# Performance work log

Measured on AMD Instinct MI355X. Metric: run time of the kernel, lower is better.

Reference implementation:

```python
import jax, jax.numpy as jnp
import numpy as np

D_MODEL = 1024
HIDDEN = 512
NUM_EXPERTS = 16
TOP_K = 2
CAP_FACTOR = 1.25
ALPHA = 0.01


def setup_inputs() -> dict:
    key = jax.random.key(0)
    ks = jax.random.split(key, 10)
    s_in = 1.0 / np.sqrt(D_MODEL)
    s_h = 1.0 / np.sqrt(HIDDEN)
    return {
        "x": jax.random.normal(ks[0], (4, 4096, D_MODEL), dtype=jnp.float32),
        "gate_w": jax.random.normal(ks[1], (D_MODEL, NUM_EXPERTS), dtype=jnp.float32) * s_in,
        "gate_b": jnp.zeros((NUM_EXPERTS,), dtype=jnp.float32),
        "gp_w": jax.random.normal(ks[2], (NUM_EXPERTS, D_MODEL, HIDDEN), dtype=jnp.float32) * s_in,
        "gp_b": jnp.zeros((NUM_EXPERTS, HIDDEN), dtype=jnp.float32),
        "up_w": jax.random.normal(ks[3], (NUM_EXPERTS, D_MODEL, HIDDEN), dtype=jnp.float32) * s_in,
        "up_b": jnp.zeros((NUM_EXPERTS, HIDDEN), dtype=jnp.float32),
        "dp_w": jax.random.normal(ks[4], (NUM_EXPERTS, HIDDEN, D_MODEL), dtype=jnp.float32) * s_h,
        "dp_b": jnp.zeros((NUM_EXPERTS, D_MODEL), dtype=jnp.float32),
    }


def reference(x, gate_w, gate_b, gp_w, gp_b, up_w, up_b, dp_w, dp_b):
    B, S, D = x.shape
    T = B * S
    xf = x.reshape(T, D)

    # --- MoEGate ---
    logits = xf @ gate_w + gate_b                      # [T, E]
    scores = jax.nn.softmax(logits, axis=-1)
    topk_w, topk_i = jax.lax.top_k(scores, TOP_K)      # [T, K]
    # norm_topk_prob=True in DeepSeekMoE
    topk_w = topk_w / (jnp.sum(topk_w, axis=-1, keepdims=True) + 1e-9)

    one_hot = jax.nn.one_hot(topk_i, NUM_EXPERTS, dtype=jnp.float32)  # [T, K, E]
    load = jnp.sum(one_hot, axis=(0, 1))               # [E]
    capacity = CAP_FACTOR * (T * TOP_K) / NUM_EXPERTS
    capacity_penalty = jnp.sum(jax.nn.relu(load - capacity)) / NUM_EXPERTS / T
    aux_loss = ALPHA * capacity_penalty

    # combine weight of expert e for each token: [T, E]
    comb = jnp.einsum("tke,tk->te", one_hot, topk_w)

    # --- dispatch/combine (dense per-expert, weighted by comb) ---
    out = jnp.zeros_like(xf)
    for e in range(NUM_EXPERTS):
        # Expert: down_proj(gate_proj(x) * silu(up_proj(x)))
        h = (xf @ gp_w[e] + gp_b[e]) * jax.nn.silu(xf @ up_w[e] + up_b[e])
        y = h @ dp_w[e] + dp_b[e]
        out = out + comb[:, e:e + 1] * y

    return out.reshape(B, S, D), aux_loss
```

## Files before the change

### kernel.cpp

```cpp
#include <hip/hip_runtime.h>
#include <hip/hip_bf16.h>
#include <math.h>

#define T_TOK 16384
#define DMODEL 1024
#define HID 512
#define NEXP 16
#define NASSIGN (T_TOK * 2)
#define HIST_BLK 64
#define TOK_PER_BLK (T_TOK / HIST_BLK)

typedef __bf16 bf16_8 __attribute__((ext_vector_type(8)));
typedef __bf16 bf16_4 __attribute__((ext_vector_type(4)));
typedef float f32_4 __attribute__((ext_vector_type(4)));

__device__ __forceinline__ void gload16(const __bf16* g, __bf16* l) {
  __builtin_amdgcn_global_load_lds(
      (const __attribute__((address_space(1))) void*)g,
      (__attribute__((address_space(3))) void*)l, 16, 0, 0);
}

__global__ __launch_bounds__(256) void gate_compute_kernel(
    const float* __restrict__ x, const float* __restrict__ gw, const float* __restrict__ gb,
    __bf16* __restrict__ xb, int* __restrict__ topk_idx, float2* __restrict__ topk_w)
{
  __shared__ __align__(16) float gws[4 * 1024 * 4];

  int tid = threadIdx.x;
#pragma unroll
  for (int i = 0; i < 16; ++i) {
    int c = i * 256 + tid;
    f32_4 v = ((const f32_4*)gw)[c];
    ((f32_4*)gws)[((c & 3) << 10) | (c >> 2)] = v;
  }
  __syncthreads();

  int wave = tid >> 6, lane = tid & 63;
  int tbase = blockIdx.x * 32 + wave * 8;

#pragma unroll 1
  for (int pass = 0; pass < 2; ++pass) {
    int t0 = tbase + pass * 4;
    const float* xr0 = x + (size_t)t0 * DMODEL;
    const float* xr1 = xr0 + DMODEL;
    const float* xr2 = xr1 + DMODEL;
    const float* xr3 = xr2 + DMODEL;
    __bf16* xw0 = xb + (size_t)t0 * DMODEL;
    __bf16* xw1 = xw0 + DMODEL;
    __bf16* xw2 = xw1 + DMODEL;
    __bf16* xw3 = xw2 + DMODEL;

    f32_4 acc0[4], acc1[4], acc2[4], acc3[4];
    {
      f32_4 z = {0.f, 0.f, 0.f, 0.f};
#pragma unroll
      for (int g = 0; g < 4; ++g) { acc0[g] = z; acc1[g] = z; acc2[g] = z; acc3[g] = z; }
    }

#pragma unroll
    for (int j = 0; j < 16; ++j) {
      int k = j * 64 + lane;
      float xv0 = xr0[k], xv1 = xr1[k], xv2 = xr2[k], xv3 = xr3[k];
      xw0[k] = (__bf16)xv0;
      xw1[k] = (__bf16)xv1;
      xw2[k] = (__bf16)xv2;
      xw3[k] = (__bf16)xv3;
      f32_4 w0 = ((const f32_4*)gws)[k];
      f32_4 w1 = ((const f32_4*)gws)[1024 + k];
      f32_4 w2 = ((const f32_4*)gws)[2048 + k];
      f32_4 w3 = ((const f32_4*)gws)[3072 + k];
      acc0[0] += xv0 * w0; acc0[1] += xv0 * w1; acc0[2] += xv0 * w2; acc0[3] += xv0 * w3;
      acc1[0] += xv1 * w0; acc1[1] += xv1 * w1; acc1[2] += xv1 * w2; acc1[3] += xv1 * w3;
      acc2[0] += xv2 * w0; acc2[1] += xv2 * w1; acc2[2] += xv2 * w2; acc2[3] += xv2 * w3;
      acc3[0] += xv3 * w0; acc3[1] += xv3 * w1; acc3[2] += xv3 * w2; acc3[3] += xv3 * w3;
    }

#pragma unroll
    for (int g = 0; g < 4; ++g)
#pragma unroll
      for (int w = 0; w < 4; ++w) {
        float v0 = acc0[g][w], v1 = acc1[g][w], v2 = acc2[g][w], v3 = acc3[g][w];
#pragma unroll
        for (int s = 32; s; s >>= 1) {
          v0 += __shfl_xor(v0, s, 64);
          v1 += __shfl_xor(v1, s, 64);
          v2 += __shfl_xor(v2, s, 64);
          v3 += __shfl_xor(v3, s, 64);
        }
        acc0[g][w] = v0; acc1[g][w] = v1; acc2[g][w] = v2; acc3[g][w] = v3;
      }

    int ti = lane & 3;
    float sc[16];
#pragma unroll
    for (int e = 0; e < 16; ++e) {
      int g = e >> 2, w = e & 3;
      float v = ti == 0 ? acc0[g][w] : ti == 1 ? acc1[g][w] : ti == 2 ? acc2[g][w] : acc3[g][w];
      sc[e] = v + gb[e];
    }
    float mx = -1e30f;
#pragma unroll
    for (int e = 0; e < 16; ++e) mx = fmaxf(mx, sc[e]);
    float Z = 0.f;
#pragma unroll
    for (int e = 0; e < 16; ++e) { sc[e] = expf(sc[e] - mx); Z += sc[e]; }
    int i0 = 0; float s0 = sc[0];
#pragma unroll
    for (int e = 1; e < 16; ++e) if (sc[e] > s0) { s0 = sc[e]; i0 = e; }
    int i1 = -1; float s1 = -1e30f;
#pragma unroll
    for (int e = 0; e < 16; ++e) if (e != i0 && sc[e] > s1) { s1 = sc[e]; i1 = e; }
    s0 /= Z; s1 /= Z;
    float dn = s0 + s1 + 1e-9f;
    if (lane < 4) {
      int t = t0 + ti;
      topk_idx[t] = i0 | (i1 << 8);
      topk_w[t] = make_float2(s0 / dn, s1 / dn);
    }
  }
}

__global__ __launch_bounds__(256) void hist_kernel(
    const int* __restrict__ topk_idx, int* __restrict__ block_hist)
{
  __shared__ int cnt[NEXP];
  int tid = threadIdx.x;
  if (tid < NEXP) cnt[tid] = 0;
  __syncthreads();
  int t = blockIdx.x * TOK_PER_BLK + tid;
  int p = topk_idx[t];
  atomicAdd(&cnt[p & 0xff], 1);
  atomicAdd(&cnt[p >> 8], 1);
  __syncthreads();
  if (tid < NEXP) block_hist[blockIdx.x * NEXP + tid] = cnt[tid];
}

__global__ void scan2_kernel(const int* __restrict__ block_hist,
                             int* __restrict__ counts, int* __restrict__ offsets,
                             int* __restrict__ block_base, float* __restrict__ aux_out)
{
  __shared__ int cl[NEXP];
  int lane = threadIdx.x;
  if (lane < NEXP) {
    int s = 0;
    for (int b = 0; b < HIST_BLK; ++b) s += block_hist[b * NEXP + lane];
    cl[lane] = s;
    counts[lane] = s;
  }
  __syncthreads();
  if (lane < NEXP) {
    int off = 0;
    for (int e = 0; e < lane; ++e) off += cl[e];
    offsets[lane] = off;
    int base = off;
    for (int b = 0; b < HIST_BLK; ++b) {
      block_base[b * NEXP + lane] = base;
      base += block_hist[b * NEXP + lane];
    }
  }
  if (lane == 0) {
    int tot = 0; float pen = 0.f;
    const float cap = 1.25f * (float)(T_TOK * 2) / (float)NEXP;
    for (int e = 0; e < NEXP; ++e) {
      tot += cl[e];
      float ld = (float)cl[e] - cap;
      pen += ld > 0.f ? ld : 0.f;
    }
    offsets[NEXP] = tot;
    aux_out[0] = 0.01f * pen / (float)NEXP / (float)T_TOK;
  }
}

__global__ __launch_bounds__(256) void scatter_kernel(
    const int* __restrict__ topk_idx, const int* __restrict__ block_base,
    int* __restrict__ tok_list, int2* __restrict__ tok_slots)
{
  __shared__ int base[NEXP];
  int tid = threadIdx.x;
  if (tid < NEXP) base[tid] = block_base[blockIdx.x * NEXP + tid];
  __syncthreads();
  int t = blockIdx.x * TOK_PER_BLK + tid;
  int p = topk_idx[t];
  int i0 = p & 0xff, i1 = p >> 8;
  int p0 = atomicAdd(&base[i0], 1);
  tok_list[p0] = t;
  int p1 = atomicAdd(&base[i1], 1);
  tok_list[p1] = t;
  tok_slots[t] = make_int2(p0, p1);
}

__global__ __launch_bounds__(256) void transpose_w1_kernel(const float* __restrict__ gp,
                                                           const float* __restrict__ up,
                                                           __bf16* __restrict__ wb1)
{
  __shared__ float tile[32][33];
  int ez = blockIdx.z;
  int e = ez >> 1, isup = ez & 1;
  const float* in = isup ? up : gp;
  int c0 = blockIdx.x * 32, r0 = blockIdx.y * 32;
  const float* src = in + ((size_t)e * 1024 + r0) * 512 + c0;
#pragma unroll
  for (int i = 0; i < 4; ++i) {
    int r = threadIdx.y + i * 8;
    tile[r][threadIdx.x] = src[(size_t)r * 512 + threadIdx.x];
  }
  __syncthreads();
#pragma unroll
  for (int i = 0; i < 4; ++i) {
    int cc = threadIdx.y + i * 8;
    int np = 2 * c0 + 2 * (cc & ~15) + (cc & 15) + 16 * isup;
    wb1[((size_t)e * 1024 + np) * 1024 + r0 + threadIdx.x] = (__bf16)tile[threadIdx.x][cc];
  }
}

__global__ __launch_bounds__(256) void transpose_dp_kernel(const float* __restrict__ in,
                                                           __bf16* __restrict__ out)
{
  __shared__ float tile[32][33];
  int e = blockIdx.z;
  int c0 = blockIdx.x * 32, r0 = blockIdx.y * 32;
  const float* src = in + ((size_t)e * 512 + r0) * 1024 + c0;
#pragma unroll
  for (int i = 0; i < 4; ++i) {
    int r = threadIdx.y + i * 8;
    tile[r][threadIdx.x] = src[(size_t)r * 1024 + threadIdx.x];
  }
  __syncthreads();
  __bf16* dst = out + ((size_t)e * 1024 + c0) * 512 + r0;
#pragma unroll
  for (int i = 0; i < 4; ++i) {
    int c = threadIdx.y + i * 8;
    dst[(size_t)c * 512 + threadIdx.x] = (__bf16)tile[threadIdx.x][c];
  }
}


#define PHASE_MID()                                          \
  __builtin_amdgcn_sched_barrier(0);                         \
  __builtin_amdgcn_s_barrier();                              \
  asm volatile("s_waitcnt lgkmcnt(0)" ::: "memory");         \
  __builtin_amdgcn_sched_barrier(0);                         \
  __builtin_amdgcn_s_setprio(1);

#define PHASE_END()                                          \
  __builtin_amdgcn_s_setprio(0);                             \
  __builtin_amdgcn_sched_barrier(0);                         \
  __builtin_amdgcn_s_barrier();

#define KTILE_BODY(STG)                                                           \
  {                                                                               \
    const __bf16* A_ = AsL + cur * 16384;                                         \
    const __bf16* B_ = BsL + cur * 16384;                                         \
    bf16_8 af[8];                                                                 \
    bf16_8 b0, b1;                                                                \
                     \
    _Pragma("unroll")                                                             \
    for (int mi = 0; mi < 8; ++mi)                                                \
      af[mi] = *(const bf16_8*)(A_ + abase + mi * 1024 + c0);                     \
    b0 = *(const bf16_8*)(B_ + bbase + c0);                                       \
    b1 = *(const bf16_8*)(B_ + bbase + 1024 + c0);                                \
    if (STG) {                                                                    \
      gload16(ga0 + koff, AsL + nxt * 16384 + tid * 8);                           \
      gload16(ga1 + koff, AsL + nxt * 16384 + 4096 + tid * 8);                    \
      gload16(ga2 + koff, AsL + nxt * 16384 + 8192 + tid * 8);                    \
      gload16(ga3 + koff, AsL + nxt * 16384 + 12288 + tid * 8);                   \
    }                                                                             \
    PHASE_MID();                                                                  \
    _Pragma("unroll")                                                             \
    for (int mi = 0; mi < 8; ++mi) {                                              \
      acc[mi][0] = __builtin_amdgcn_mfma_f32_16x16x32_bf16(af[mi], b0, acc[mi][0], 0, 0, 0); \
      acc[mi][1] = __builtin_amdgcn_mfma_f32_16x16x32_bf16(af[mi], b1, acc[mi][1], 0, 0, 0); \
    }                                                                             \
    PHASE_END();                                                                  \
                                       \
    b0 = *(const bf16_8*)(B_ + bbase + 2048 + c0);                                \
    b1 = *(const bf16_8*)(B_ + bbase + 3072 + c0);                                \
    if (STG) {                                                                    \
      gload16(gb0 + koff, BsL + nxt * 16384 + tid * 8);                           \
      gload16(gb1 + koff, BsL + nxt * 16384 + 4096 + tid * 8);                    \
      gload16(gb2 + koff, BsL + nxt * 16384 + 8192 + tid * 8);                    \
      gload16(gb3 + koff, BsL + nxt * 16384 + 12288 + tid * 8);                   \
    }                                                                             \
    PHASE_MID();                                                                  \
    _Pragma("unroll")                                                             \
    for (int mi = 0; mi < 8; ++mi) {                                              \
      acc[mi][2] = __builtin_amdgcn_mfma_f32_16x16x32_bf16(af[mi], b0, acc[mi][2], 0, 0, 0); \
      acc[mi][3] = __builtin_amdgcn_mfma_f32_16x16x32_bf16(af[mi], b1, acc[mi][3], 0, 0, 0); \
    }                                                                             \
    PHASE_END();                                                                  \
                                     \
    _Pragma("unroll")                                                             \
    for (int mi = 0; mi < 8; ++mi)                                                \
      af[mi] = *(const bf16_8*)(A_ + abase + mi * 1024 + (c0 ^ 32));              \
    b0 = *(const bf16_8*)(B_ + bbase + (c0 ^ 32));                                \
    b1 = *(const bf16_8*)(B_ + bbase + 1024 + (c0 ^ 32));                         \
    PHASE_MID();                                                                  \
    _Pragma("unroll")                                                             \
    for (int mi = 0; mi < 8; ++mi) {                                              \
      acc[mi][0] = __builtin_amdgcn_mfma_f32_16x16x32_bf16(af[mi], b0, acc[mi][0], 0, 0, 0); \
      acc[mi][1] = __builtin_amdgcn_mfma_f32_16x16x32_bf16(af[mi], b1, acc[mi][1], 0, 0, 0); \
    }                                                                             \
    PHASE_END();                                                                  \
          \
    b0 = *(const bf16_8*)(B_ + bbase + 2048 + (c0 ^ 32));                         \
    b1 = *(const bf16_8*)(B_ + bbase + 3072 + (c0 ^ 32));                         \
    if (STG) { asm volatile("s_waitcnt vmcnt(0)" ::: "memory"); }                 \
    PHASE_MID();                                                                  \
    _Pragma("unroll")                                                             \
    for (int mi = 0; mi < 8; ++mi) {                                              \
      acc[mi][2] = __builtin_amdgcn_mfma_f32_16x16x32_bf16(af[mi], b0, acc[mi][2], 0, 0, 0); \
      acc[mi][3] = __builtin_amdgcn_mfma_f32_16x16x32_bf16(af[mi], b1, acc[mi][3], 0, 0, 0); \
    }                                                                             \
    PHASE_END();                                                                  \
  }

template<int KTILES>
__device__ __forceinline__ void gemm8w(
    const __bf16* ga0, const __bf16* ga1, const __bf16* ga2, const __bf16* ga3,
    const __bf16* gb0, const __bf16* gb1, const __bf16* gb2, const __bf16* gb3,
    __bf16* AsL, __bf16* BsL, f32_4 (&acc)[8][4])
{
  int tid = threadIdx.x;
  int wid = tid >> 6, wr = wid >> 2, wc = wid & 3;
  int lane = tid & 63, quad = lane >> 4, l16 = lane & 15;
  int c0 = ((quad ^ (l16 & 7)) * 8);
  int abase = (wr * 128 + l16) * 64;
  int bbase = (wc * 64 + l16) * 64;

  gload16(ga0, AsL + tid * 8);
  gload16(ga1, AsL + 4096 + tid * 8);
  gload16(ga2, AsL + 8192 + tid * 8);
  gload16(ga3, AsL + 12288 + tid * 8);
  gload16(gb0, BsL + tid * 8);
  gload16(gb1, BsL + 4096 + tid * 8);
  gload16(gb2, BsL + 8192 + tid * 8);
  gload16(gb3, BsL + 12288 + tid * 8);
  __syncthreads();

  int cur = 0;
#pragma unroll 1
  for (int kt = 0; kt < KTILES - 1; ++kt) {
    int nxt = cur ^ 1;
    int koff = (kt + 1) * 64;
    KTILE_BODY(1);
    cur = nxt;
  }
  {
    int nxt = 0; int koff = 0;
    KTILE_BODY(0);
  }
}

__global__ __launch_bounds__(512, 2) void ffn1_kernel(
    const __bf16* __restrict__ xb, const __bf16* __restrict__ wb1,
    const float* __restrict__ gp_b, const float* __restrict__ up_b,
    const int* __restrict__ counts, const int* __restrict__ offsets,
    const int* __restrict__ tok_list, __bf16* __restrict__ h)
{
  int e = blockIdx.z;
  int cnt = counts[e];
  int m0 = blockIdx.y * 256;
  if (m0 >= cnt) return;
  int n0 = blockIdx.x * 256;
  int offe = offsets[e];

  __shared__ __align__(16) __bf16 As[2][256 * 64];
  __shared__ __align__(16) __bf16 Bs[2][256 * 64];
  __shared__ int toks[256];

  int tid = threadIdx.x;
  if (tid < 256) {
    int r = m0 + tid;
    toks[tid] = tok_list[offe + (r < cnt ? r : cnt - 1)];
  }
  __syncthreads();

  int rr = tid >> 3;
  int ko = ((tid & 7) ^ (rr & 7)) * 8;

  f32_4 acc[8][4];
  {
    f32_4 z = {0.f, 0.f, 0.f, 0.f};
#pragma unroll
    for (int a = 0; a < 8; ++a)
#pragma unroll
      for (int b = 0; b < 4; ++b) acc[a][b] = z;
  }

  gemm8w<DMODEL / 64>(
      xb + (size_t)toks[rr] * DMODEL + ko,
      xb + (size_t)toks[64 + rr] * DMODEL + ko,
      xb + (size_t)toks[128 + rr] * DMODEL + ko,
      xb + (size_t)toks[192 + rr] * DMODEL + ko,
      wb1 + ((size_t)e * 1024 + n0 + rr) * DMODEL + ko,
      wb1 + ((size_t)e * 1024 + n0 + 64 + rr) * DMODEL + ko,
      wb1 + ((size_t)e * 1024 + n0 + 128 + rr) * DMODEL + ko,
      wb1 + ((size_t)e * 1024 + n0 + 192 + rr) * DMODEL + ko,
      &As[0][0], &Bs[0][0], acc);

  int wid = tid >> 6, wr = wid >> 2, wc = wid & 3;
  int lane = tid & 63, quad = lane >> 4, l16 = lane & 15;

#pragma unroll
  for (int mi = 0; mi < 8; ++mi)
#pragma unroll
    for (int j = 0; j < 2; ++j) {
      int c = (n0 >> 1) + wc * 32 + j * 16 + l16;
      float gbias = gp_b[e * HID + c];
      float ubias = up_b[e * HID + c];
#pragma unroll
      for (int rg = 0; rg < 4; ++rg) {
        int r = m0 + wr * 128 + mi * 16 + quad * 4 + rg;
        if (r < cnt) {
          float g = acc[mi][2 * j][rg] + gbias;
          float u = acc[mi][2 * j + 1][rg] + ubias;
          float sw = u / (1.f + expf(-u));
          h[(size_t)(offe + r) * HID + c] = (__bf16)(g * sw);
        }
      }
    }
}

__global__ __launch_bounds__(512, 2) void ffn2_kernel(
    const __bf16* __restrict__ h, const __bf16* __restrict__ dpb, const float* __restrict__ dp_b,
    const int* __restrict__ counts, const int* __restrict__ offsets,
    __bf16* __restrict__ ybuf)
{
  int e = blockIdx.z;
  int cnt = counts[e];
  int m0 = blockIdx.y * 256;
  if (m0 >= cnt) return;
  int n0 = blockIdx.x * 256;
  int offe = offsets[e];

  __shared__ __align__(16) __bf16 As[2][256 * 64];
  __shared__ __align__(16) __bf16 Bs[2][256 * 64];

  int tid = threadIdx.x;
  int rr = tid >> 3;
  int ko = ((tid & 7) ^ (rr & 7)) * 8;

  int ra0 = m0 + rr;        if (ra0 >= cnt) ra0 = cnt - 1;
  int ra1 = m0 + 64 + rr;   if (ra1 >= cnt) ra1 = cnt - 1;
  int ra2 = m0 + 128 + rr;  if (ra2 >= cnt) ra2 = cnt - 1;
  int ra3 = m0 + 192 + rr;  if (ra3 >= cnt) ra3 = cnt - 1;

  f32_4 acc[8][4];
  {
    f32_4 z = {0.f, 0.f, 0.f, 0.f};
#pragma unroll
    for (int a = 0; a < 8; ++a)
#pragma unroll
      for (int b = 0; b < 4; ++b) acc[a][b] = z;
  }

  gemm8w<HID / 64>(
      h + (size_t)(offe + ra0) * HID + ko,
      h + (size_t)(offe + ra1) * HID + ko,
      h + (size_t)(offe + ra2) * HID + ko,
      h + (size_t)(offe + ra3) * HID + ko,
      dpb + ((size_t)e * DMODEL + n0 + rr) * HID + ko,
      dpb + ((size_t)e * DMODEL + n0 + 64 + rr) * HID + ko,
      dpb + ((size_t)e * DMODEL + n0 + 128 + rr) * HID + ko,
      dpb + ((size_t)e * DMODEL + n0 + 192 + rr) * HID + ko,
      &As[0][0], &Bs[0][0], acc);

  int wid = tid >> 6, wr = wid >> 2, wc = wid & 3;
  int lane = tid & 63, quad = lane >> 4, l16 = lane & 15;

#pragma unroll
  for (int mi = 0; mi < 8; ++mi)
#pragma unroll
    for (int ni = 0; ni < 4; ++ni) {
      int n = n0 + wc * 64 + ni * 16 + l16;
      float bias = dp_b[e * DMODEL + n];
#pragma unroll
      for (int rg = 0; rg < 4; ++rg) {
        int r = m0 + wr * 128 + mi * 16 + quad * 4 + rg;
        if (r < cnt) {
          float v = acc[mi][ni][rg] + bias;
          ybuf[(size_t)(offe + r) * DMODEL + n] = (__bf16)v;
        }
      }
    }
}

__global__ __launch_bounds__(256) void combine_kernel(
    const __bf16* __restrict__ ybuf, const int2* __restrict__ tok_slots,
    const float2* __restrict__ topk_w, float* __restrict__ out)
{
  int tid = threadIdx.x;
  int t = blockIdx.x * 2 + (tid >> 7);
  int d = (tid & 127) * 8;
  int2 sl = tok_slots[t];
  float2 w = topk_w[t];
  bf16_8 y0 = *(const bf16_8*)(ybuf + (size_t)sl.x * DMODEL + d);
  bf16_8 y1 = *(const bf16_8*)(ybuf + (size_t)sl.y * DMODEL + d);
  float* o = out + (size_t)t * DMODEL + d;
  f32_4 r0, r1;
#pragma unroll
  for (int i = 0; i < 4; ++i) r0[i] = w.x * (float)y0[i] + w.y * (float)y1[i];
#pragma unroll
  for (int i = 0; i < 4; ++i) r1[i] = w.x * (float)y0[4 + i] + w.y * (float)y1[4 + i];
  *(f32_4*)o = r0;
  *(f32_4*)(o + 4) = r1;
}

extern "C" void kernel_launch(void* const* d_in, const int* in_sizes, int n_in,
                              void* d_out, int out_size, void* d_ws, size_t ws_size,
                              hipStream_t stream)
{
  const float* x      = (const float*)d_in[0];
  const float* gate_w = (const float*)d_in[1];
  const float* gate_b = (const float*)d_in[2];
  const float* gp_w   = (const float*)d_in[3];
  const float* gp_b   = (const float*)d_in[4];
  const float* up_w   = (const float*)d_in[5];
  const float* up_b   = (const float*)d_in[6];
  const float* dp_w   = (const float*)d_in[7];
  const float* dp_b   = (const float*)d_in[8];

  char* ws = (char*)d_ws;
  size_t o = 0;
  __bf16* xb  = (__bf16*)(ws + o); o += (size_t)T_TOK * DMODEL * 2;
  __bf16* wb1 = (__bf16*)(ws + o); o += (size_t)NEXP * 1024 * DMODEL * 2;
  __bf16* dpb = (__bf16*)(ws + o); o += (size_t)NEXP * DMODEL * HID * 2;
  __bf16* hbuf = (__bf16*)(ws + o); o += (size_t)NASSIGN * HID * 2;
  int*   tok_list = (int*)(ws + o); o += (size_t)NASSIGN * 4;
  int2*  tok_slots = (int2*)(ws + o); o += (size_t)T_TOK * 8;
  int*   topk_idx = (int*)(ws + o); o += (size_t)T_TOK * 4;
  float2* topk_w  = (float2*)(ws + o); o += (size_t)T_TOK * 8;
  int*   block_hist = (int*)(ws + o); o += (size_t)HIST_BLK * NEXP * 4;
  int*   block_base = (int*)(ws + o); o += (size_t)HIST_BLK * NEXP * 4;
  int*   counts   = (int*)(ws + o); o += 64;
  int*   offsets  = (int*)(ws + o); o += 128;
  __bf16* ybuf = (__bf16*)ws;

  float* out = (float*)d_out;
  float* aux = out + (size_t)T_TOK * DMODEL;

  gate_compute_kernel<<<T_TOK / 32, 256, 0, stream>>>(x, gate_w, gate_b, xb, topk_idx, topk_w);
  hist_kernel<<<HIST_BLK, TOK_PER_BLK, 0, stream>>>(topk_idx, block_hist);
  scan2_kernel<<<1, 64, 0, stream>>>(block_hist, counts, offsets, block_base, aux);
  scatter_kernel<<<HIST_BLK, TOK_PER_BLK, 0, stream>>>(topk_idx, block_base, tok_list, tok_slots);
  transpose_w1_kernel<<<dim3(512 / 32, 1024 / 32, 2 * NEXP), dim3(32, 8), 0, stream>>>(gp_w, up_w, wb1);
  transpose_dp_kernel<<<dim3(1024 / 32, 512 / 32, NEXP), dim3(32, 8), 0, stream>>>(dp_w, dpb);
  ffn1_kernel<<<dim3(1024 / 256, NASSIGN / 256, NEXP), 512, 0, stream>>>(xb, wb1, gp_b, up_b,
                                                                         counts, offsets, tok_list, hbuf);
  ffn2_kernel<<<dim3(DMODEL / 256, NASSIGN / 256, NEXP), 512, 0, stream>>>(hbuf, dpb, dp_b,
                                                                           counts, offsets, ybuf);
  combine_kernel<<<T_TOK / 2, 256, 0, stream>>>(ybuf, tok_slots, topk_w, out);
}
```

Measured before the change: 460.8 us.

## Use compact M-block table, XCD-aware grid mapping and 4-stage K32 GEMM pipeline

The scan kernel now builds a compact table of (expert, m-block) pairs, so the FFN kernels launch a dense grid instead of a sparse 3D grid with many early-exit blocks. Block indices are remapped so that work is grouped per XCD, which aims to improve L2 reuse. The GEMM core switches from a 2-stage pipeline with K=64 tiles to a 4-buffer pipeline with K=32 tiles, staging three tiles ahead with finer vmcnt waits so memory latency overlaps better with compute. The cost is more barriers per unit of K, and the hardcoded 72/71 XCD split relies on NMB_MAX=143.

```diff
diff --git a/kernel.cpp b/kernel.cpp
--- a/kernel.cpp
+++ b/kernel.cpp
@@ -9,6 +9,7 @@
 #define NASSIGN (T_TOK * 2)
 #define HIST_BLK 64
 #define TOK_PER_BLK (T_TOK / HIST_BLK)
+#define NMB_MAX 143
 
 typedef __bf16 bf16_8 __attribute__((ext_vector_type(8)));
 typedef __bf16 bf16_4 __attribute__((ext_vector_type(4)));
@@ -137,7 +138,8 @@
 
 __global__ void scan2_kernel(const int* __restrict__ block_hist,
                              int* __restrict__ counts, int* __restrict__ offsets,
-                             int* __restrict__ block_base, float* __restrict__ aux_out)
+                             int* __restrict__ block_base, int* __restrict__ mb_tab,
+                             int* __restrict__ nmb, float* __restrict__ aux_out)
 {
   __shared__ int cl[NEXP];
   int lane = threadIdx.x;
@@ -168,6 +170,12 @@
     }
     offsets[NEXP] = tot;
     aux_out[0] = 0.01f * pen / (float)NEXP / (float)T_TOK;
+    int idx = 0;
+    for (int e = 0; e < NEXP; ++e) {
+      int nb = (cl[e] + 255) >> 8;
+      for (int b = 0; b < nb; ++b) mb_tab[idx++] = (e << 8) | b;
+    }
+    nmb[0] = idx;
   }
 }
 
@@ -247,126 +255,103 @@
   __builtin_amdgcn_sched_barrier(0);                         \
   __builtin_amdgcn_s_barrier();
 
-#define KTILE_BODY(STG)                                                           \
+#define MF(mi, ni, a, b) acc[mi][ni] = __builtin_amdgcn_mfma_f32_16x16x32_bf16(a, b, acc[mi][ni], 0, 0, 0)
+
+#define STAGE_A(b, kt) {                                       \
+    gload16(ga0 + (kt) * 32, lds + (b) * 16384 + tid * 8);     \
+    gload16(ga1 + (kt) * 32, lds + (b) * 16384 + 4096 + tid * 8); }
+#define STAGE_B(b, kt) {                                       \
+    gload16(gb0 + (kt) * 32, lds + (b) * 16384 + 8192 + tid * 8); \
+    gload16(gb1 + (kt) * 32, lds + (b) * 16384 + 12288 + tid * 8); }
+
+#define GTILE(ktv, STG, ENDVM)                                                    \
   {                                                                               \
-    const __bf16* A_ = AsL + cur * 16384;                                         \
-    const __bf16* B_ = BsL + cur * 16384;                                         \
-    bf16_8 af[8];                                                                 \
-    bf16_8 b0, b1;                                                                \
-                     \
-    _Pragma("unroll")                                                             \
-    for (int mi = 0; mi < 8; ++mi)                                                \
-      af[mi] = *(const bf16_8*)(A_ + abase + mi * 1024 + c0);                     \
-    b0 = *(const bf16_8*)(B_ + bbase + c0);                                       \
-    b1 = *(const bf16_8*)(B_ + bbase + 1024 + c0);                                \
-    if (STG) {                                                                    \
-      gload16(ga0 + koff, AsL + nxt * 16384 + tid * 8);                           \
-      gload16(ga1 + koff, AsL + nxt * 16384 + 4096 + tid * 8);                    \
-      gload16(ga2 + koff, AsL + nxt * 16384 + 8192 + tid * 8);                    \
-      gload16(ga3 + koff, AsL + nxt * 16384 + 12288 + tid * 8);                   \
-    }                                                                             \
+    const __bf16* A_ = lds + ((ktv) & 3) * 16384;                                 \
+    const __bf16* B_ = A_ + 8192;                                                 \
+    bf16_8 af0, af1, af2, af3, bf0, bf1, bf2, bf3;                                \
+    af0 = *(const bf16_8*)(A_ + abase + 0 * 512 + aq);                            \
+    af1 = *(const bf16_8*)(A_ + abase + 1 * 512 + aq);                            \
+    af2 = *(const bf16_8*)(A_ + abase + 2 * 512 + aq);                            \
+    af3 = *(const bf16_8*)(A_ + abase + 3 * 512 + aq);                            \
+    bf0 = *(const bf16_8*)(B_ + bbase + 0 * 512 + aq);                            \
+    bf1 = *(const bf16_8*)(B_ + bbase + 1 * 512 + aq);                            \
+    bf2 = *(const bf16_8*)(B_ + bbase + 2 * 512 + aq);                            \
+    bf3 = *(const bf16_8*)(B_ + bbase + 3 * 512 + aq);                            \
+    if (STG) STAGE_A(((ktv) + 3) & 3, (ktv) + 3);                                 \
     PHASE_MID();                                                                  \
-    _Pragma("unroll")                                                             \
-    for (int mi = 0; mi < 8; ++mi) {                                              \
-      acc[mi][0] = __builtin_amdgcn_mfma_f32_16x16x32_bf16(af[mi], b0, acc[mi][0], 0, 0, 0); \
-      acc[mi][1] = __builtin_amdgcn_mfma_f32_16x16x32_bf16(af[mi], b1, acc[mi][1], 0, 0, 0); \
-    }                                                                             \
+    MF(0, 0, af0, bf0); MF(0, 1, af0, bf1); MF(0, 2, af0, bf2); MF(0, 3, af0, bf3); \
+    MF(1, 0, af1, bf0); MF(1, 1, af1, bf1); MF(1, 2, af1, bf2); MF(1, 3, af1, bf3); \
+    MF(2, 0, af2, bf0); MF(2, 1, af2, bf1); MF(2, 2, af2, bf2); MF(2, 3, af2, bf3); \
+    MF(3, 0, af3, bf0); MF(3, 1, af3, bf1); MF(3, 2, af3, bf2); MF(3, 3, af3, bf3); \
     PHASE_END();                                                                  \
-                                       \
-    b0 = *(const bf16_8*)(B_ + bbase + 2048 + c0);                                \
-    b1 = *(const bf16_8*)(B_ + bbase + 3072 + c0);                                \
-    if (STG) {                                                                    \
-      gload16(gb0 + koff, BsL + nxt * 16384 + tid * 8);                           \
-      gload16(gb1 + koff, BsL + nxt * 16384 + 4096 + tid * 8);                    \
-      gload16(gb2 + koff, BsL + nxt * 16384 + 8192 + tid * 8);                    \
-      gload16(gb3 + koff, BsL + nxt * 16384 + 12288 + tid * 8);                   \
-    }                                                                             \
+    af0 = *(const bf16_8*)(A_ + abase + 4 * 512 + aq);                            \
+    af1 = *(const bf16_8*)(A_ + abase + 5 * 512 + aq);                            \
+    af2 = *(const bf16_8*)(A_ + abase + 6 * 512 + aq);                            \
+    af3 = *(const bf16_8*)(A_ + abase + 7 * 512 + aq);                            \
+    if (STG) STAGE_B(((ktv) + 3) & 3, (ktv) + 3);                                 \
     PHASE_MID();                                                                  \
-    _Pragma("unroll")                                                             \
-    for (int mi = 0; mi < 8; ++mi) {                                              \
-      acc[mi][2] = __builtin_amdgcn_mfma_f32_16x16x32_bf16(af[mi], b0, acc[mi][2], 0, 0, 0); \
-      acc[mi][3] = __builtin_amdgcn_mfma_f32_16x16x32_bf16(af[mi], b1, acc[mi][3], 0, 0, 0); \
-    }                                                                             \
-    PHASE_END();                                                                  \
-                                     \
-    _Pragma("unroll")                                                             \
-    for (int mi = 0; mi < 8; ++mi)                                                \
-      af[mi] = *(const bf16_8*)(A_ + abase + mi * 1024 + (c0 ^ 32));              \
-    b0 = *(const bf16_8*)(B_ + bbase + (c0 ^ 32));                                \
-    b1 = *(const bf16_8*)(B_ + bbase + 1024 + (c0 ^ 32));                         \
-    PHASE_MID();                                                                  \
-    _Pragma("unroll")                                                             \
-    for (int mi = 0; mi < 8; ++mi) {                                              \
-      acc[mi][0] = __builtin_amdgcn_mfma_f32_16x16x32_bf16(af[mi], b0, acc[mi][0], 0, 0, 0); \
-      acc[mi][1] = __builtin_amdgcn_mfma_f32_16x16x32_bf16(af[mi], b1, acc[mi][1], 0, 0, 0); \
-    }                                                                             \
-    PHASE_END();                                                                  \
-          \
-    b0 = *(const bf16_8*)(B_ + bbase + 2048 + (c0 ^ 32));                         \
-    b1 = *(const bf16_8*)(B_ + bbase + 3072 + (c0 ^ 32));                         \
-    if (STG) { asm volatile("s_waitcnt vmcnt(0)" ::: "memory"); }                 \
-    PHASE_MID();                                                                  \
-    _Pragma("unroll")                                                             \
-    for (int mi = 0; mi < 8; ++mi) {                                              \
-      acc[mi][2] = __builtin_amdgcn_mfma_f32_16x16x32_bf16(af[mi], b0, acc[mi][2], 0, 0, 0); \
-      acc[mi][3] = __builtin_amdgcn_mfma_f32_16x16x32_bf16(af[mi], b1, acc[mi][3], 0, 0, 0); \
-    }                                                                             \
-    PHASE_END();                                                                  \
+    MF(4, 0, af0, bf0); MF(4, 1, af0, bf1); MF(4, 2, af0, bf2); MF(4, 3, af0, bf3); \
+    MF(5, 0, af1, bf0); MF(5, 1, af1, bf1); MF(5, 2, af1, bf2); MF(5, 3, af1, bf3); \
+    MF(6, 0, af2, bf0); MF(6, 1, af2, bf1); MF(6, 2, af2, bf2); MF(6, 3, af2, bf3); \
+    MF(7, 0, af3, bf0); MF(7, 1, af3, bf1); MF(7, 2, af3, bf2); MF(7, 3, af3, bf3); \
+    __builtin_amdgcn_s_setprio(0);                                                \
+    __builtin_amdgcn_sched_barrier(0);                                            \
+    if ((ENDVM) == 8)      asm volatile("s_waitcnt vmcnt(8)" ::: "memory");       \
+    else if ((ENDVM) == 4) asm volatile("s_waitcnt vmcnt(4)" ::: "memory");       \
+    else if ((ENDVM) == 0) asm volatile("s_waitcnt vmcnt(0)" ::: "memory");       \
+    __builtin_amdgcn_sched_barrier(0);                                            \
+    __builtin_amdgcn_s_barrier();                                                 \
   }
 
 template<int KTILES>
 __device__ __forceinline__ void gemm8w(
-    const __bf16* ga0, const __bf16* ga1, const __bf16* ga2, const __bf16* ga3,
-    const __bf16* gb0, const __bf16* gb1, const __bf16* gb2, const __bf16* gb3,
-    __bf16* AsL, __bf16* BsL, f32_4 (&acc)[8][4])
-{
-  int tid = threadIdx.x;
-  int wid = tid >> 6, wr = wid >> 2, wc = wid & 3;
-  int lane = tid & 63, quad = lane >> 4, l16 = lane & 15;
-  int c0 = ((quad ^ (l16 & 7)) * 8);
-  int abase = (wr * 128 + l16) * 64;
-  int bbase = (wc * 64 + l16) * 64;
-
-  gload16(ga0, AsL + tid * 8);
-  gload16(ga1, AsL + 4096 + tid * 8);
-  gload16(ga2, AsL + 8192 + tid * 8);
-  gload16(ga3, AsL + 12288 + tid * 8);
-  gload16(gb0, BsL + tid * 8);
-  gload16(gb1, BsL + 4096 + tid * 8);
-  gload16(gb2, BsL + 8192 + tid * 8);
-  gload16(gb3, BsL + 12288 + tid * 8);
-  __syncthreads();
-
-  int cur = 0;
+    const __bf16* ga0, const __bf16* ga1,
+    const __bf16* gb0, const __bf16* gb1,
+    __bf16* lds, f32_4 (&acc)[8][4])
+{
+  const int tid = threadIdx.x;
+  const int wid = tid >> 6, wr = wid >> 2, wc = wid & 3;
+  const int lane = tid & 63, quad = lane >> 4, l16 = lane & 15;
+  const int aq = (quad ^ (l16 & 3)) * 8;
+  const int abase = (wr * 128 + l16) * 32;
+  const int bbase = (wc * 64 + l16) * 32;
+
+  STAGE_A(0, 0); STAGE_B(0, 0);
+  STAGE_A(1, 1); STAGE_B(1, 1);
+  STAGE_A(2, 2); STAGE_B(2, 2);
+  asm volatile("s_waitcnt vmcnt(8)" ::: "memory");
+  __builtin_amdgcn_sched_barrier(0);
+  __builtin_amdgcn_s_barrier();
+
 #pragma unroll 1
-  for (int kt = 0; kt < KTILES - 1; ++kt) {
-    int nxt = cur ^ 1;
-    int koff = (kt + 1) * 64;
-    KTILE_BODY(1);
-    cur = nxt;
-  }
-  {
-    int nxt = 0; int koff = 0;
-    KTILE_BODY(0);
-  }
+  for (int kt = 0; kt < KTILES - 3; ++kt) {
+    GTILE(kt, 1, 8);
+  }
+  GTILE(KTILES - 3, 0, 4);
+  GTILE(KTILES - 2, 0, 0);
+  GTILE(KTILES - 1, 0, -1);
 }
 
 __global__ __launch_bounds__(512, 2) void ffn1_kernel(
     const __bf16* __restrict__ xb, const __bf16* __restrict__ wb1,
     const float* __restrict__ gp_b, const float* __restrict__ up_b,
     const int* __restrict__ counts, const int* __restrict__ offsets,
-    const int* __restrict__ tok_list, __bf16* __restrict__ h)
-{
-  int e = blockIdx.z;
-  int cnt = counts[e];
-  int m0 = blockIdx.y * 256;
-  if (m0 >= cnt) return;
-  int n0 = blockIdx.x * 256;
-  int offe = offsets[e];
-
-  __shared__ __align__(16) __bf16 As[2][256 * 64];
-  __shared__ __align__(16) __bf16 Bs[2][256 * 64];
+    const int* __restrict__ tok_list, const int* __restrict__ mb_tab,
+    const int* __restrict__ nmb, __bf16* __restrict__ h)
+{
+  __shared__ __align__(16) __bf16 lds[4 * 16384];
   __shared__ int toks[256];
+
+  int lin = blockIdx.y * 4 + blockIdx.x;
+  int xcd = lin & 7, sub = lin >> 3;
+  int wg = (xcd < 4 ? xcd * 72 : 288 + (xcd - 4) * 71) + sub;
+  int y = wg >> 2, xn = wg & 3;
+  if (y >= nmb[0]) return;
+  int me = mb_tab[y];
+  int e = me >> 8;
+  int m0 = (me & 255) << 8;
+  int cnt = counts[e], offe = offsets[e];
+  int n0 = xn * 256;
 
   int tid = threadIdx.x;
   if (tid < 256) {
@@ -375,8 +360,13 @@
   }
   __syncthreads();
 
-  int rr = tid >> 3;
-  int ko = ((tid & 7) ^ (rr & 7)) * 8;
+  int rr = tid >> 2;
+  int ko = ((tid & 3) ^ (rr & 3)) * 8;
+
+  const __bf16* ga0 = xb + (size_t)toks[rr] * DMODEL + ko;
+  const __bf16* ga1 = xb + (size_t)toks[128 + rr] * DMODEL + ko;
+  const __bf16* gb0 = wb1 + ((size_t)e * 1024 + n0 + rr) * DMODEL + ko;
+  const __bf16* gb1 = wb1 + ((size_t)e * 1024 + n0 + 128 + rr) * DMODEL + ko;
 
   f32_4 acc[8][4];
   {
@@ -387,16 +377,7 @@
       for (int b = 0; b < 4; ++b) acc[a][b] = z;
   }
 
-  gemm8w<DMODEL / 64>(
-      xb + (size_t)toks[rr] * DMODEL + ko,
-      xb + (size_t)toks[64 + rr] * DMODEL + ko,
-      xb + (size_t)toks[128 + rr] * DMODEL + ko,
-      xb + (size_t)toks[192 + rr] * DMODEL + ko,
-      wb1 + ((size_t)e * 1024 + n0 + rr) * DMODEL + ko,
-      wb1 + ((size_t)e * 1024 + n0 + 64 + rr) * DMODEL + ko,
-      wb1 + ((size_t)e * 1024 + n0 + 128 + rr) * DMODEL + ko,
-      wb1 + ((size_t)e * 1024 + n0 + 192 + rr) * DMODEL + ko,
-      &As[0][0], &Bs[0][0], acc);
+  gemm8w<DMODEL / 32>(ga0, ga1, gb0, gb1, lds, acc);
 
   int wid = tid >> 6, wr = wid >> 2, wc = wid & 3;
   int lane = tid & 63, quad = lane >> 4, l16 = lane & 15;
@@ -424,26 +405,32 @@
 __global__ __launch_bounds__(512, 2) void ffn2_kernel(
     const __bf16* __restrict__ h, const __bf16* __restrict__ dpb, const float* __restrict__ dp_b,
     const int* __restrict__ counts, const int* __restrict__ offsets,
+    const int* __restrict__ mb_tab, const int* __restrict__ nmb,
     __bf16* __restrict__ ybuf)
 {
-  int e = blockIdx.z;
-  int cnt = counts[e];
-  int m0 = blockIdx.y * 256;
-  if (m0 >= cnt) return;
-  int n0 = blockIdx.x * 256;
-  int offe = offsets[e];
-
-  __shared__ __align__(16) __bf16 As[2][256 * 64];
-  __shared__ __align__(16) __bf16 Bs[2][256 * 64];
+  __shared__ __align__(16) __bf16 lds[4 * 16384];
+
+  int lin = blockIdx.y * 4 + blockIdx.x;
+  int xcd = lin & 7, sub = lin >> 3;
+  int wg = (xcd < 4 ? xcd * 72 : 288 + (xcd - 4) * 71) + sub;
+  int y = wg >> 2, xn = wg & 3;
+  if (y >= nmb[0]) return;
+  int me = mb_tab[y];
+  int e = me >> 8;
+  int m0 = (me & 255) << 8;
+  int cnt = counts[e], offe = offsets[e];
+  int n0 = xn * 256;
 
   int tid = threadIdx.x;
-  int rr = tid >> 3;
-  int ko = ((tid & 7) ^ (rr & 7)) * 8;
+  int rr = tid >> 2;
+  int ko = ((tid & 3) ^ (rr & 3)) * 8;
 
   int ra0 = m0 + rr;        if (ra0 >= cnt) ra0 = cnt - 1;
-  int ra1 = m0 + 64 + rr;   if (ra1 >= cnt) ra1 = cnt - 1;
-  int ra2 = m0 + 128 + rr;  if (ra2 >= cnt) ra2 = cnt - 1;
-  int ra3 = m0 + 192 + rr;  if (ra3 >= cnt) ra3 = cnt - 1;
+  int ra1 = m0 + 128 + rr;  if (ra1 >= cnt) ra1 = cnt - 1;
+  const __bf16* ga0 = h + (size_t)(offe + ra0) * HID + ko;
+  const __bf16* ga1 = h + (size_t)(offe + ra1) * HID + ko;
+  const __bf16* gb0 = dpb + ((size_t)e * DMODEL + n0 + rr) * HID + ko;
+  const __bf16* gb1 = dpb + ((size_t)e * DMODEL + n0 + 128 + rr) * HID + ko;
 
   f32_4 acc[8][4];
   {
@@ -454,16 +441,7 @@
       for (int b = 0; b < 4; ++b) acc[a][b] = z;
   }
 
-  gemm8w<HID / 64>(
-      h + (size_t)(offe + ra0) * HID + ko,
-      h + (size_t)(offe + ra1) * HID + ko,
-      h + (size_t)(offe + ra2) * HID + ko,
-      h + (size_t)(offe + ra3) * HID + ko,
-      dpb + ((size_t)e * DMODEL + n0 + rr) * HID + ko,
-      dpb + ((size_t)e * DMODEL + n0 + 64 + rr) * HID + ko,
-      dpb + ((size_t)e * DMODEL + n0 + 128 + rr) * HID + ko,
-      dpb + ((size_t)e * DMODEL + n0 + 192 + rr) * HID + ko,
-      &As[0][0], &Bs[0][0], acc);
+  gemm8w<HID / 32>(ga0, ga1, gb0, gb1, lds, acc);
 
   int wid = tid >> 6, wr = wid >> 2, wc = wid & 3;
   int lane = tid & 63, quad = lane >> 4, l16 = lane & 15;
@@ -534,6 +512,8 @@
   int*   block_base = (int*)(ws + o); o += (size_t)HIST_BLK * NEXP * 4;
   int*   counts   = (int*)(ws + o); o += 64;
   int*   offsets  = (int*)(ws + o); o += 128;
+  int*   mb_tab   = (int*)(ws + o); o += 4 * 160;
+  int*   nmb      = (int*)(ws + o); o += 64;
   __bf16* ybuf = (__bf16*)ws;
 
   float* out = (float*)d_out;
@@ -541,13 +521,13 @@
 
   gate_compute_kernel<<<T_TOK / 32, 256, 0, stream>>>(x, gate_w, gate_b, xb, topk_idx, topk_w);
   hist_kernel<<<HIST_BLK, TOK_PER_BLK, 0, stream>>>(topk_idx, block_hist);
-  scan2_kernel<<<1, 64, 0, stream>>>(block_hist, counts, offsets, block_base, aux);
+  scan2_kernel<<<1, 64, 0, stream>>>(block_hist, counts, offsets, block_base, mb_tab, nmb, aux);
   scatter_kernel<<<HIST_BLK, TOK_PER_BLK, 0, stream>>>(topk_idx, block_base, tok_list, tok_slots);
   transpose_w1_kernel<<<dim3(512 / 32, 1024 / 32, 2 * NEXP), dim3(32, 8), 0, stream>>>(gp_w, up_w, wb1);
   transpose_dp_kernel<<<dim3(1024 / 32, 512 / 32, NEXP), dim3(32, 8), 0, stream>>>(dp_w, dpb);
-  ffn1_kernel<<<dim3(1024 / 256, NASSIGN / 256, NEXP), 512, 0, stream>>>(xb, wb1, gp_b, up_b,
-                                                                         counts, offsets, tok_list, hbuf);
-  ffn2_kernel<<<dim3(DMODEL / 256, NASSIGN / 256, NEXP), 512, 0, stream>>>(hbuf, dpb, dp_b,
-                                                                           counts, offsets, ybuf);
+  ffn1_kernel<<<dim3(4, NMB_MAX, 1), 512, 0, stream>>>(xb, wb1, gp_b, up_b,
+                                                       counts, offsets, tok_list, mb_tab, nmb, hbuf);
+  ffn2_kernel<<<dim3(4, NMB_MAX, 1), 512, 0, stream>>>(hbuf, dpb, dp_b,
+                                                       counts, offsets, mb_tab, nmb, ybuf);
   combine_kernel<<<T_TOK / 2, 256, 0, stream>>>(ybuf, tok_slots, topk_w, out);
 }
```

New measurement: 486.6 us. 1.06x slower.
